# Performance work log

Measured on AMD Instinct MI355X. Metric: run time of the kernel, lower is better.

Reference implementation:

```python
import jax, jax.numpy as jnp
import numpy as np

# hyperparameters (match init_kwargs / AF3 atom transformer)
B, N, C, CP = 1, 2048, 128, 16      # batch, n_atom, c_atom, c_atom_pair
H, D = 4, 32                        # heads, head dim
HD = H * D                          # 128
NB = 3                              # no_blocks
TC = 2 * C                          # n_transition * c_atom
NQ, NK = 32, 128                    # n_query, n_key
INF = 1.0e9


def _ln(x, g=None, b=None):
    m = jnp.mean(x, axis=-1, keepdims=True)
    v = jnp.mean((x - m) ** 2, axis=-1, keepdims=True)
    y = (x - m) * jax.lax.rsqrt(v + 1e-5)
    if g is not None:
        y = y * g
    if b is not None:
        y = y + b
    return y


def _adaln(a, s, gamma, wsig, bsig, wskip):
    # AF3 Algorithm 26: AdaLN(a, s)
    an = _ln(a)                     # no affine
    sn = _ln(s, gamma)              # scale only
    return jax.nn.sigmoid(sn @ wsig + bsig) * an + sn @ wskip


def _neighborhood_beta():
    # compute_neighborhood_mask with create_sparsity_mask=False
    n_center = N // NQ + 1
    centers = (NQ / 2 - 0.5) + jnp.arange(n_center, dtype=jnp.float32) * NQ
    l = jnp.arange(N, dtype=jnp.float32)
    row = (jnp.abs(l[:, None] - centers[None, :]) < NQ / 2).astype(jnp.float32)
    col = (jnp.abs(l[:, None] - centers[None, :]) < NK / 2).astype(jnp.float32)
    beta = row @ col.T              # [N, N], in {0,1} since query windows are disjoint
    return (beta - 1.0) * INF       # 0 where attended, -inf elsewhere


def setup_inputs() -> dict:
    key = jax.random.key(0)
    it = iter(jax.random.split(key, 64))
    def rn(shape, s=0.02):
        return jax.random.normal(next(it), shape, jnp.float32) * s
    inp = dict(
        ql=rn((B, N, C), 1.0),
        cl=rn((B, N, C), 1.0),
        plm=rn((B, N, N, CP), 1.0),
        atom_mask=jnp.ones((B, N), jnp.float32),
        # per-block stacked params, leading dim NB
        attn_gamma=1.0 + rn((NB, C)), attn_wsig=rn((NB, C, C)),
        attn_bsig=rn((NB, C)), attn_wskip=rn((NB, C, C)),
        wq=rn((NB, C, HD)), bq=rn((NB, HD)), wk=rn((NB, C, HD)), wv=rn((NB, C, HD)),
        lnz_g=1.0 + rn((NB, CP)), lnz_b=rn((NB, CP)), w_pair=rn((NB, CP, H)),
        w_gate=rn((NB, C, HD)), w_out=rn((NB, HD, C)),
        w_ao=rn((NB, C, C)), b_ao=rn((NB, C)) - 2.0,
        tr_gamma=1.0 + rn((NB, C)), tr_wsig=rn((NB, C, C)),
        tr_bsig=rn((NB, C)), tr_wskip=rn((NB, C, C)),
        w_t1=rn((NB, C, TC)), w_t2=rn((NB, C, TC)), w_t3=rn((NB, TC, C)),
        w_to=rn((NB, C, C)), b_to=rn((NB, C)) - 2.0,
    )
    return inp


def reference(ql, cl, plm, atom_mask,
              attn_gamma, attn_wsig, attn_bsig, attn_wskip,
              wq, bq, wk, wv, lnz_g, lnz_b, w_pair,
              w_gate, w_out, w_ao, b_ao,
              tr_gamma, tr_wsig, tr_bsig, tr_wskip,
              w_t1, w_t2, w_t3, w_to, b_to):
    beta = _neighborhood_beta()                       # [N, N]
    mask_bias = (atom_mask - 1.0) * INF               # [B, N]
    scale = 1.0 / np.sqrt(D)
    a, s = ql, cl
    for i in range(NB):
        # --- AttentionPairBias with AdaLN (AF3 Alg. 24) ---
        an = _adaln(a, s, attn_gamma[i], attn_wsig[i], attn_bsig[i], attn_wskip[i])
        q = (an @ wq[i] + bq[i]).reshape(B, N, H, D)
        k = (an @ wk[i]).reshape(B, N, H, D)
        v = (an @ wv[i]).reshape(B, N, H, D)
        pb = _ln(plm, lnz_g[i], lnz_b[i]) @ w_pair[i]  # [B, N, N, H]
        logits = (jnp.einsum('bqhd,bkhd->bhqk', q, k) * scale
                  + pb.transpose(0, 3, 1, 2)
                  + beta[None, None]
                  + mask_bias[:, None, None, :])
        attn = jax.nn.softmax(logits, axis=-1)
        o = jnp.einsum('bhqk,bkhd->bqhd', attn, v)
        g = jax.nn.sigmoid(an @ w_gate[i]).reshape(B, N, H, D)
        o = (g * o).reshape(B, N, HD) @ w_out[i]
        b_attn = jax.nn.sigmoid(s @ w_ao[i] + b_ao[i]) * o   # adaLN-zero output gate
        # --- ConditionedTransitionBlock (AF3 Alg. 25) on old a ---
        tn = _adaln(a, s, tr_gamma[i], tr_wsig[i], tr_bsig[i], tr_wskip[i])
        t = jax.nn.silu(tn @ w_t1[i]) * (tn @ w_t2[i])       # SwiGLU
        t = jax.nn.sigmoid(s @ w_to[i] + b_to[i]) * (t @ w_t3[i])
        a = b_attn + t                                       # AF3 Alg. 23
    return a
```

## Files before the change

kernel.cpp:

```cpp
#include <hip/hip_runtime.h>
#include <math.h>

#define NA 2048
#define CD 128
#define NC ((size_t)262144)

typedef unsigned short u16;
typedef short s8v __attribute__((ext_vector_type(8)));
typedef float f4v __attribute__((ext_vector_type(4)));
#define MFMA __builtin_amdgcn_mfma_f32_16x16x32_bf16

__device__ __forceinline__ float sigm(float x) { return 1.f / (1.f + __expf(-x)); }
__device__ __forceinline__ u16 f2bf(float x) {
    unsigned u = __float_as_uint(x);
    u += 0x7fffu + ((u >> 16) & 1u);
    return (u16)(u >> 16);
}
__device__ __forceinline__ float bf2f(u16 h) { return __uint_as_float((unsigned)h << 16); }

__global__ __launch_bounds__(256)
void prep_w(const float* __restrict__ attn_gamma, const float* __restrict__ attn_wsig,
            const float* __restrict__ attn_bsig, const float* __restrict__ attn_wskip,
            const float* __restrict__ wq, const float* __restrict__ wk,
            const float* __restrict__ wv, const float* __restrict__ w_gate,
            const float* __restrict__ w_out, const float* __restrict__ w_ao,
            const float* __restrict__ b_ao,
            const float* __restrict__ tr_gamma, const float* __restrict__ tr_wsig,
            const float* __restrict__ tr_bsig, const float* __restrict__ tr_wskip,
            const float* __restrict__ w_t1, const float* __restrict__ w_t2,
            const float* __restrict__ w_t3, const float* __restrict__ w_to,
            const float* __restrict__ b_to,
            u16* __restrict__ BP1h, u16* __restrict__ BP1l,
            u16* __restrict__ BG1h, u16* __restrict__ BG1l,
            u16* __restrict__ BG2h, u16* __restrict__ BG2l,
            float* __restrict__ Pbias) {
    int e = blockIdx.x * 256 + threadIdx.x;
    if (e >= 835584) {
        int t = e - 835584;
        if (t < 2304) {
            int z = t / 768, rem = t % 768, j = rem >> 7, c = rem & 127;
            float v = 0.f;
            if (j == 0) v = attn_bsig[z * 128 + c];
            else if (j == 2) v = tr_bsig[z * 128 + c];
            else if (j == 4) v = b_ao[z * 128 + c];
            else if (j == 5) v = b_to[z * 128 + c];
            Pbias[t] = v;
        }
        return;
    }
    int z = e / 278528, r = e % 278528;
    float val;
    u16 *dh, *dl;
    size_t dofs;
    if (r < 98304) {
        int c = r >> 7, k = r & 127, seg = c >> 7, cc = c & 127;
        const float* w;
        const float* g = nullptr;
        switch (seg) {
            case 0: w = attn_wsig; g = attn_gamma; break;
            case 1: w = attn_wskip; g = attn_gamma; break;
            case 2: w = tr_wsig; g = tr_gamma; break;
            case 3: w = tr_wskip; g = tr_gamma; break;
            case 4: w = w_ao; break;
            default: w = w_to; break;
        }
        val = w[((size_t)z * 128 + k) * 128 + cc];
        if (g) val *= g[z * 128 + k];
        dh = BP1h; dl = BP1l; dofs = (size_t)z * 98304 + r;
    } else if (r < 229376) {
        int t = r - 98304, c = t >> 7, k = t & 127;
        if (c < 512) {
            int seg = c >> 7, cc = c & 127;
            const float* w = (seg == 0) ? wq : (seg == 1) ? wk : (seg == 2) ? wv : w_gate;
            val = w[((size_t)z * 128 + k) * 128 + cc];
        } else {
            int tt = c - 512;
            const float* w = (tt < 256) ? w_t1 : w_t2;
            val = w[(size_t)z * 32768 + (size_t)k * 256 + (tt & 255)];
        }
        dh = BG1h; dl = BG1l; dofs = (size_t)z * 131072 + t;
    } else {
        int t = r - 229376, c = t / 384, k = t % 384;
        val = (k < 128) ? w_out[((size_t)z * 128 + k) * 128 + c]
                        : w_t3[(size_t)z * 32768 + (size_t)(k - 128) * 128 + c];
        dh = BG2h; dl = BG2l; dofs = (size_t)z * 49152 + t;
    }
    u16 h = f2bf(val);
    dh[dofs] = h;
    dl[dofs] = f2bf(val - bf2f(h));
}

__global__ __launch_bounds__(256)
void pb_kernel(const float* __restrict__ plm, const float* __restrict__ lnz_g,
               const float* __restrict__ lnz_b, const float* __restrict__ w_pair,
               float* __restrict__ pb) {
    __shared__ float gw[3][4][16];
    __shared__ float c0s[3][4];
    int t = threadIdx.x;
    if (t < 12) {
        int i = t >> 2, h = t & 3;
        float c = 0.f;
        for (int cp = 0; cp < 16; ++cp) {
            float wp = w_pair[(i * 16 + cp) * 4 + h];
            gw[i][h][cp] = lnz_g[i * 16 + cp] * wp;
            c += lnz_b[i * 16 + cp] * wp;
        }
        c0s[i][h] = c;
    }
    __syncthreads();
    int c = blockIdx.x;
    int p = blockIdx.y * 256 + t;
    int ql = p >> 7, kl = p & 127;
    int kstart = max(0, c * 32 - 48), kend = min(2048, c * 32 + 80);
    int k = kstart + kl;
    if (k >= kend) {
#pragma unroll
        for (int i = 0; i < 3; ++i)
#pragma unroll
            for (int h = 0; h < 4; ++h)
                pb[((((size_t)i * 64 + c) * 4 + h) * 32 + ql) * 128 + kl] = 0.f;
        return;
    }
    int q = c * 32 + ql;
    const float* row = plm + ((size_t)q * 2048 + (size_t)k) * 16;
    float x[16];
#pragma unroll
    for (int j = 0; j < 4; ++j) {
        float4 v = *(const float4*)(row + j * 4);
        x[j * 4 + 0] = v.x; x[j * 4 + 1] = v.y; x[j * 4 + 2] = v.z; x[j * 4 + 3] = v.w;
    }
    float s = 0.f, sq = 0.f;
#pragma unroll
    for (int cp = 0; cp < 16; ++cp) { s += x[cp]; sq += x[cp] * x[cp]; }
    float mean = s * (1.f / 16.f);
    float var = sq * (1.f / 16.f) - mean * mean;
    float r = 1.f / sqrtf(var + 1e-5f);
    float xn[16];
#pragma unroll
    for (int cp = 0; cp < 16; ++cp) xn[cp] = (x[cp] - mean) * r;
#pragma unroll
    for (int i = 0; i < 3; ++i)
#pragma unroll
        for (int h = 0; h < 4; ++h) {
            float d = c0s[i][h];
#pragma unroll
            for (int cp = 0; cp < 16; ++cp) d = fmaf(xn[cp], gw[i][h][cp], d);
            pb[((((size_t)i * 64 + c) * 4 + h) * 32 + ql) * 128 + kl] = d;
        }
}

__global__ __launch_bounds__(256)
void mf_p1f(const float* __restrict__ cl, const u16* __restrict__ B1h, const u16* __restrict__ B1l,
            const float* __restrict__ Pbias, float* __restrict__ sg) {
    const int r0 = blockIdx.x * 32, chunk = blockIdx.y, z = blockIdx.z;
    __shared__ u16 Ah[32 * 128], Al[32 * 128];
    {
        const int tid = threadIdx.x;
        const int row = tid >> 3, cb = (tid & 7) * 16;
        const float* ar = cl + (size_t)(r0 + row) * CD + cb;
        float x[16];
#pragma unroll
        for (int j = 0; j < 4; ++j) {
            float4 v = *(const float4*)(ar + j * 4);
            x[4 * j] = v.x; x[4 * j + 1] = v.y; x[4 * j + 2] = v.z; x[4 * j + 3] = v.w;
        }
        float s = 0.f, sq = 0.f;
#pragma unroll
        for (int j = 0; j < 16; ++j) { s += x[j]; sq += x[j] * x[j]; }
#pragma unroll
        for (int m = 1; m < 8; m <<= 1) { s += __shfl_xor(s, m); sq += __shfl_xor(sq, m); }
        float mean = s * (1.f / 128.f), var = sq * (1.f / 128.f) - mean * mean;
        float rr = 1.f / sqrtf(var + 1e-5f);
#pragma unroll
        for (int gp = 0; gp < 2; ++gp) {
            u16 hv8[8], lv8[8];
#pragma unroll
            for (int j = 0; j < 8; ++j) {
                float xv = x[gp * 8 + j];
                float val = (chunk < 4) ? (xv - mean) * rr : xv;
                u16 hh = f2bf(val);
                hv8[j] = hh; lv8[j] = f2bf(val - bf2f(hh));
            }
            int g = ((cb >> 3) + gp) ^ (row & 7);
            *(s8v*)(Ah + row * 128 + g * 8) = *(s8v*)hv8;
            *(s8v*)(Al + row * 128 + g * 8) = *(s8v*)lv8;
        }
    }
    __syncthreads();
    const int l = threadIdx.x & 63, w = threadIdx.x >> 6;
    const int lr = l & 15, lq = l >> 4, kg = lq * 8;
    const int c0 = w * 32;
    const u16* Bh = B1h + (size_t)z * 98304 + (size_t)chunk * 16384;
    const u16* Bl = B1l + (size_t)z * 98304 + (size_t)chunk * 16384;
    f4v acc[2][2] = {};
#pragma unroll
    for (int ks = 0; ks < 4; ++ks) {
        int g = (4 * ks + lq) ^ (lr & 7);
        s8v a0h = *(const s8v*)(Ah + lr * 128 + g * 8);
        s8v a1h = *(const s8v*)(Ah + (16 + lr) * 128 + g * 8);
        s8v a0l = *(const s8v*)(Al + lr * 128 + g * 8);
        s8v a1l = *(const s8v*)(Al + (16 + lr) * 128 + g * 8);
        s8v b0h = *(const s8v*)(Bh + (size_t)(c0 + lr) * 128 + ks * 32 + kg);
        s8v b1h = *(const s8v*)(Bh + (size_t)(c0 + 16 + lr) * 128 + ks * 32 + kg);
        s8v b0l = *(const s8v*)(Bl + (size_t)(c0 + lr) * 128 + ks * 32 + kg);
        s8v b1l = *(const s8v*)(Bl + (size_t)(c0 + 16 + lr) * 128 + ks * 32 + kg);
        acc[0][0] = MFMA(a0h, b0h, acc[0][0], 0, 0, 0); acc[0][1] = MFMA(a0h, b1h, acc[0][1], 0, 0, 0);
        acc[1][0] = MFMA(a1h, b0h, acc[1][0], 0, 0, 0); acc[1][1] = MFMA(a1h, b1h, acc[1][1], 0, 0, 0);
        acc[0][0] = MFMA(a0h, b0l, acc[0][0], 0, 0, 0); acc[0][1] = MFMA(a0h, b1l, acc[0][1], 0, 0, 0);
        acc[1][0] = MFMA(a1h, b0l, acc[1][0], 0, 0, 0); acc[1][1] = MFMA(a1h, b1l, acc[1][1], 0, 0, 0);
        acc[0][0] = MFMA(a0l, b0h, acc[0][0], 0, 0, 0); acc[0][1] = MFMA(a0l, b1h, acc[0][1], 0, 0, 0);
        acc[1][0] = MFMA(a1l, b0h, acc[1][0], 0, 0, 0); acc[1][1] = MFMA(a1l, b1h, acc[1][1], 0, 0, 0);
    }
    const bool dosig = (chunk != 1) && (chunk != 3);
    const float* bp = Pbias + (z * 6 + chunk) * 128;
    float* dst = sg + ((size_t)z * 6 + chunk) * NC;
#pragma unroll
    for (int mi = 0; mi < 2; ++mi)
#pragma unroll
        for (int i = 0; i < 4; ++i) {
            int row = r0 + mi * 16 + lq * 4 + i;
#pragma unroll
            for (int ni = 0; ni < 2; ++ni) {
                int col = c0 + ni * 16 + lr;
                float xx = acc[mi][ni][i];
                if (dosig) xx = sigm(xx + bp[col]);
                dst[(size_t)row * CD + col] = xx;
            }
        }
}

__global__ __launch_bounds__(256)
void k1_fused(const float* __restrict__ a, const float* __restrict__ sgi,
              const u16* __restrict__ B1h, const u16* __restrict__ B1l,
              const float* __restrict__ bq,
              u16* __restrict__ qgh, u16* __restrict__ qgl,
              u16* __restrict__ vTh, u16* __restrict__ vTl,
              float* __restrict__ tbuf) {
    const int r0 = blockIdx.x * 32;
    const int y = blockIdx.y;
    __shared__ u16 Ah[32 * 128], Al[32 * 128];
    {
        const int tid = threadIdx.x;
        const int row = tid >> 3, cb = (tid & 7) * 16;
        const float* ar = a + (size_t)(r0 + row) * CD + cb;
        float x[16];
#pragma unroll
        for (int j = 0; j < 4; ++j) {
            float4 v = *(const float4*)(ar + j * 4);
            x[4 * j] = v.x; x[4 * j + 1] = v.y; x[4 * j + 2] = v.z; x[4 * j + 3] = v.w;
        }
        float s = 0.f, sq = 0.f;
#pragma unroll
        for (int j = 0; j < 16; ++j) { s += x[j]; sq += x[j] * x[j]; }
#pragma unroll
        for (int m = 1; m < 8; m <<= 1) { s += __shfl_xor(s, m); sq += __shfl_xor(sq, m); }
        float mean = s * (1.f / 128.f), var = sq * (1.f / 128.f) - mean * mean;
        float rr = 1.f / sqrtf(var + 1e-5f);
        const float* sig = sgi + ((y < 2) ? 0 : 2 * NC) + (size_t)(r0 + row) * CD + cb;
        const float* skp = sgi + ((y < 2) ? NC : 3 * NC) + (size_t)(r0 + row) * CD + cb;
// ... 2 lines not shown
            u16 hv8[8], lv8[8];
#pragma unroll
            for (int j = 0; j < 8; ++j) {
                int jj = gp * 8 + j;
                float ln = (x[jj] - mean) * rr;
                float val = fmaf(sig[jj], ln, skp[jj]);
                u16 hh = f2bf(val);
                hv8[j] = hh; lv8[j] = f2bf(val - bf2f(hh));
            }
            int g = ((cb >> 3) + gp) ^ (row & 7);
            *(s8v*)(Ah + row * 128 + g * 8) = *(s8v*)hv8;
            *(s8v*)(Al + row * 128 + g * 8) = *(s8v*)lv8;
        }
    }
    __syncthreads();
    const int l = threadIdx.x & 63, w = threadIdx.x >> 6;
    const int lr = l & 15, lq = l >> 4, kg = lq * 8;
    const int chunk = 2 * y + (w >> 1);
    const int cbase = (w & 1) * 64;
    f4v acc[2][2][2] = {};
#pragma unroll
    for (int ks = 0; ks < 4; ++ks) {
        int g = (4 * ks + lq) ^ (lr & 7);
        s8v a0h = *(const s8v*)(Ah + lr * 128 + g * 8);
        s8v a1h = *(const s8v*)(Ah + (16 + lr) * 128 + g * 8);
        s8v a0l = *(const s8v*)(Al + lr * 128 + g * 8);
        s8v a1l = *(const s8v*)(Al + (16 + lr) * 128 + g * 8);
#pragma unroll
        for (int t2 = 0; t2 < 2; ++t2) {
            int crow = chunk * 128 + cbase + t2 * 32;
            s8v b0h = *(const s8v*)(B1h + (size_t)(crow + lr) * 128 + ks * 32 + kg);
            s8v b1h = *(const s8v*)(B1h + (size_t)(crow + 16 + lr) * 128 + ks * 32 + kg);
            s8v b0l = *(const s8v*)(B1l + (size_t)(crow + lr) * 128 + ks * 32 + kg);
            s8v b1l = *(const s8v*)(B1l + (size_t)(crow + 16 + lr) * 128 + ks * 32 + kg);
// ... 10 lines not shown
            acc[t2][1][0] = MFMA(a1l, b0h, acc[t2][1][0], 0, 0, 0);
            acc[t2][1][1] = MFMA(a1l, b1h, acc[t2][1][1], 0, 0, 0);
        }
    }
#pragma unroll
    for (int t2 = 0; t2 < 2; ++t2)
#pragma unroll
        for (int mi = 0; mi < 2; ++mi)
#pragma unroll
            for (int i = 0; i < 4; ++i) {
                int row = r0 + mi * 16 + lq * 4 + i;
#pragma unroll
                for (int ni = 0; ni < 2; ++ni) {
                    int gcol = chunk * 128 + cbase + t2 * 32 + ni * 16 + lr;
                    float x = acc[t2][mi][ni][i];
                    if (chunk == 0) x += bq[gcol];
                    if (gcol < 512) {
                        u16 hh = f2bf(x), ll = f2bf(x - bf2f(hh));
                        qgh[(size_t)row * 512 + gcol] = hh;
                        qgl[(size_t)row * 512 + gcol] = ll;
                        if (chunk == 2) {
                            int cv = gcol - 256;
                            vTh[(size_t)cv * 2048 + row] = hh;
                            vTl[(size_t)cv * 2048 + row] = ll;
                        }
                    } else {
                        tbuf[(size_t)row * 512 + (gcol - 512)] = x;
                    }
                }
            }
}

__global__ __launch_bounds__(64)
void attn_mfma(const u16* __restrict__ qgh, const u16* __restrict__ qgl,
               const u16* __restrict__ vTh, const u16* __restrict__ vTl,
               const float* __restrict__ pb, const float* __restrict__ atom_mask,
               u16* __restrict__ ogh, u16* __restrict__ ogl) {
    const int c = blockIdx.x, h = blockIdx.y;
    const int l = threadIdx.x;
    const int kstart = max(0, c * 32 - 48);
    const int kend = min(2048, c * 32 + 80);
    const int nk = kend - kstart;
    const int lr = l & 15, lq = l >> 4, kg = lq * 8;

    __shared__ u16 Pls[32 * 128];

    s8v qfh[2], qfl[2];
#pragma unroll
    for (int mi = 0; mi < 2; ++mi) {
        size_t qb = (size_t)(c * 32 + mi * 16 + lr) * 512 + h * 32 + kg;
        qfh[mi] = *(const s8v*)(qgh + qb);
        qfl[mi] = *(const s8v*)(qgl + qb);
    }
    f4v lac[2][8] = {};
#pragma unroll
    for (int kt = 0; kt < 8; ++kt) {
        int krow = min(kstart + kt * 16 + lr, 2047);
        size_t kb = (size_t)krow * 512 + 128 + h * 32 + kg;
        s8v bh = *(const s8v*)(qgh + kb);
        s8v bl = *(const s8v*)(qgl + kb);
        lac[0][kt] = MFMA(qfh[0], bh, lac[0][kt], 0, 0, 0);
        lac[1][kt] = MFMA(qfh[1], bh, lac[1][kt], 0, 0, 0);
        lac[0][kt] = MFMA(qfh[0], bl, lac[0][kt], 0, 0, 0);
        lac[1][kt] = MFMA(qfh[1], bl, lac[1][kt], 0, 0, 0);
        lac[0][kt] = MFMA(qfl[0], bh, lac[0][kt], 0, 0, 0);
        lac[1][kt] = MFMA(qfl[1], bh, lac[1][kt], 0, 0, 0);
    }
    float mb8[8];
#pragma unroll
    for (int kt = 0; kt < 8; ++kt) {
        int kl = kt * 16 + lr;
        mb8[kt] = (kl < nk) ? (atom_mask[kstart + kl] - 1.f) * 1.0e9f : 0.f;
    }
    const float scale = 0.17677669529663687f;
    const float* pbp = pb + (size_t)((c * 4 + h) * 32) * 128;
    float inv_s[2][4];
#pragma unroll
    for (int mi = 0; mi < 2; ++mi)
#pragma unroll
        for (int i = 0; i < 4; ++i) {
            const int rl = mi * 16 + lq * 4 + i;
            float lg[8];
#pragma unroll
            for (int kt = 0; kt < 8; ++kt) {
                int kl = kt * 16 + lr;
                float v = -1e30f;
                if (kl < nk) v = fmaf(lac[mi][kt][i], scale, pbp[(size_t)rl * 128 + kl] + mb8[kt]);
                lg[kt] = v;
            }
            float m = lg[0];
#pragma unroll
            for (int kt = 1; kt < 8; ++kt) m = fmaxf(m, lg[kt]);
#pragma unroll
            for (int msk = 1; msk < 16; msk <<= 1) m = fmaxf(m, __shfl_xor(m, msk));
            float ssum = 0.f;
#pragma unroll
            for (int kt = 0; kt < 8; ++kt) {
                float p = __expf(lg[kt] - m);
                u16 p16 = f2bf(p);
                ssum += bf2f(p16);
                int kl = kt * 16 + lr;
                int g = (kl >> 3) ^ (rl & 7);
                Pls[rl * 128 + g * 8 + (kl & 7)] = p16;
            }
#pragma unroll
            for (int msk = 1; msk < 16; msk <<= 1) ssum += __shfl_xor(ssum, msk);
            inv_s[mi][i] = 1.f / ssum;
        }
    __syncthreads();
    f4v oac[2][2] = {};
#pragma unroll
    for (int ks = 0; ks < 4; ++ks) {
        s8v pA[2];
#pragma unroll
        for (int mi = 0; mi < 2; ++mi) {
            int row = mi * 16 + lr;
            int g = (4 * ks + lq) ^ (row & 7);
            pA[mi] = *(const s8v*)(Pls + row * 128 + g * 8);
        }
#pragma unroll
        for (int ct = 0; ct < 2; ++ct) {
            size_t vb = (size_t)(h * 32 + ct * 16 + lr) * 2048 + kstart + ks * 32 + kg;
            s8v vh = *(const s8v*)(vTh + vb);
            s8v vl = *(const s8v*)(vTl + vb);
            oac[0][ct] = MFMA(pA[0], vh, oac[0][ct], 0, 0, 0);
            oac[1][ct] = MFMA(pA[1], vh, oac[1][ct], 0, 0, 0);
            oac[0][ct] = MFMA(pA[0], vl, oac[0][ct], 0, 0, 0);
            oac[1][ct] = MFMA(pA[1], vl, oac[1][ct], 0, 0, 0);
        }
    }
#pragma unroll
    for (int mi = 0; mi < 2; ++mi)
#pragma unroll
        for (int ct = 0; ct < 2; ++ct)
#pragma unroll
            for (int i = 0; i < 4; ++i) {
                int rl = mi * 16 + lq * 4 + i;
                int row = c * 32 + rl;
                int d = ct * 16 + lr;
                float o = oac[mi][ct][i] * inv_s[mi][i];
                size_t gidx = (size_t)row * 512 + 384 + h * 32 + d;
                float g = bf2f(qgh[gidx]) + bf2f(qgl[gidx]);
                float v = o * sigm(g);
                u16 hh = f2bf(v);
                size_t oi = (size_t)row * 128 + h * 32 + d;
                ogh[oi] = hh;
                ogl[oi] = f2bf(v - bf2f(hh));
            }
}

__global__ __launch_bounds__(256)
void k3_fused(const float* __restrict__ tbuf,
              const u16* __restrict__ ogh, const u16* __restrict__ ogl,
              const u16* __restrict__ B2h, const u16* __restrict__ B2l,
              const float* __restrict__ sg4, const float* __restrict__ sg5,
              float* __restrict__ dst) {
    const int r0 = blockIdx.x * 32;
    __shared__ u16 Sh[32 * 256], Sl[32 * 256];
    {
        const int tid = threadIdx.x;
        const int row = tid >> 3, cb = (tid & 7) * 32;
#pragma unroll
        for (int u = 0; u < 4; ++u) {
            int colb = cb + u * 8;
            const float* t1 = tbuf + (size_t)(r0 + row) * 512 + colb;
            const float* t2 = t1 + 256;
            u16 hv8[8], lv8[8];
#pragma unroll
            for (int j2 = 0; j2 < 2; ++j2) {
                float4 x1 = *(const float4*)(t1 + j2 * 4);
                float4 x2 = *(const float4*)(t2 + j2 * 4);
                float sv[4];
                sv[0] = x1.x * sigm(x1.x) * x2.x;
                sv[1] = x1.y * sigm(x1.y) * x2.y;
                sv[2] = x1.z * sigm(x1.z) * x2.z;
                sv[3] = x1.w * sigm(x1.w) * x2.w;
#pragma unroll
                for (int j = 0; j < 4; ++j) {
                    u16 hh = f2bf(sv[j]);
                    hv8[j2 * 4 + j] = hh;
                    lv8[j2 * 4 + j] = f2bf(sv[j] - bf2f(hh));
                }
            }
            int g = (colb >> 3) ^ (row & 7);
            *(s8v*)(Sh + row * 256 + g * 8) = *(s8v*)hv8;
            *(s8v*)(Sl + row * 256 + g * 8) = *(s8v*)lv8;
        }
    }
    __syncthreads();
    const int l = threadIdx.x & 63, w = threadIdx.x >> 6;
    const int lr = l & 15, lq = l >> 4, kg = lq * 8;
    const int c0 = w * 32;
    f4v ac1[2][2] = {}, ac2[2][2] = {};
#pragma unroll
    for (int ks = 0; ks < 4; ++ks) {
        s8v a0h = *(const s8v*)(ogh + (size_t)(r0 + lr) * 128 + ks * 32 + kg);
        s8v a1h = *(const s8v*)(ogh + (size_t)(r0 + 16 + lr) * 128 + ks * 32 + kg);
        s8v a0l = *(const s8v*)(ogl + (size_t)(r0 + lr) * 128 + ks * 32 + kg);
        s8v a1l = *(const s8v*)(ogl + (size_t)(r0 + 16 + lr) * 128 + ks * 32 + kg);
        s8v b0h = *(const s8v*)(B2h + (size_t)(c0 + lr) * 384 + ks * 32 + kg);
        s8v b1h = *(const s8v*)(B2h + (size_t)(c0 + 16 + lr) * 384 + ks * 32 + kg);
        s8v b0l = *(const s8v*)(B2l + (size_t)(c0 + lr) * 384 + ks * 32 + kg);
        s8v b1l = *(const s8v*)(B2l + (size_t)(c0 + 16 + lr) * 384 + ks * 32 + kg);
        ac1[0][0] = MFMA(a0h, b0h, ac1[0][0], 0, 0, 0); ac1[0][1] = MFMA(a0h, b1h, ac1[0][1], 0, 0, 0);
        ac1[1][0] = MFMA(a1h, b0h, ac1[1][0], 0, 0, 0); ac1[1][1] = MFMA(a1h, b1h, ac1[1][1], 0, 0, 0);
        ac1[0][0] = MFMA(a0h, b0l, ac1[0][0], 0, 0, 0); ac1[0][1] = MFMA(a0h, b1l, ac1[0][1], 0, 0, 0);
        ac1[1][0] = MFMA(a1h, b0l, ac1[1][0], 0, 0, 0); ac1[1][1] = MFMA(a1h, b1l, ac1[1][1], 0, 0, 0);
        ac1[0][0] = MFMA(a0l, b0h, ac1[0][0], 0, 0, 0); ac1[0][1] = MFMA(a0l, b1h, ac1[0][1], 0, 0, 0);
        ac1[1][0] = MFMA(a1l, b0h, ac1[1][0], 0, 0, 0); ac1[1][1] = MFMA(a1l, b1h, ac1[1][1], 0, 0, 0);
    }
#pragma unroll
    for (int ks = 0; ks < 8; ++ks) {
        int g = (4 * ks + lq) ^ (lr & 7);
        s8v a0h = *(const s8v*)(Sh + lr * 256 + g * 8);
// ... 11 lines not shown
        ac2[0][0] = MFMA(a0l, b0h, ac2[0][0], 0, 0, 0); ac2[0][1] = MFMA(a0l, b1h, ac2[0][1], 0, 0, 0);
        ac2[1][0] = MFMA(a1l, b0h, ac2[1][0], 0, 0, 0); ac2[1][1] = MFMA(a1l, b1h, ac2[1][1], 0, 0, 0);
    }
#pragma unroll
    for (int mi = 0; mi < 2; ++mi)
#pragma unroll
        for (int i = 0; i < 4; ++i) {
            int row = r0 + mi * 16 + lq * 4 + i;
#pragma unroll
            for (int ni = 0; ni < 2; ++ni) {
                int col = c0 + ni * 16 + lr;
                size_t idx = (size_t)row * CD + col;
                dst[idx] = sg4[idx] * ac1[mi][ni][i] + sg5[idx] * ac2[mi][ni][i];
            }
        }
}

extern "C" void kernel_launch(void* const* d_in, const int* in_sizes, int n_in,
                              void* d_out, int out_size, void* d_ws, size_t ws_size,
                              hipStream_t stream) {
    const float* ql = (const float*)d_in[0];
    const float* cl = (const float*)d_in[1];
    const float* plm = (const float*)d_in[2];
    const float* atom_mask = (const float*)d_in[3];
    const float* attn_gamma = (const float*)d_in[4];
    const float* attn_wsig = (const float*)d_in[5];
    const float* attn_bsig = (const float*)d_in[6];
    const float* attn_wskip = (const float*)d_in[7];
    const float* wq = (const float*)d_in[8];
    const float* bq = (const float*)d_in[9];
    const float* wk = (const float*)d_in[10];
    const float* wv = (const float*)d_in[11];
    const float* lnz_g = (const float*)d_in[12];
    const float* lnz_b = (const float*)d_in[13];
    const float* w_pair = (const float*)d_in[14];
    const float* w_gate = (const float*)d_in[15];
    const float* w_out = (const float*)d_in[16];
    const float* w_ao = (const float*)d_in[17];
    const float* b_ao = (const float*)d_in[18];
    const float* tr_gamma = (const float*)d_in[19];
    const float* tr_wsig = (const float*)d_in[20];
    const float* tr_bsig = (const float*)d_in[21];
    const float* tr_wskip = (const float*)d_in[22];
    const float* w_t1 = (const float*)d_in[23];
    const float* w_t2 = (const float*)d_in[24];
    const float* w_t3 = (const float*)d_in[25];
    const float* w_to = (const float*)d_in[26];
    const float* b_to = (const float*)d_in[27];
    float* out = (float*)d_out;
    float* ws = (float*)d_ws;

    float* sg = ws;
    float* tbuf = ws + 18 * NC;
    float* pb = ws + 22 * NC;
    float* a_buf = ws + 34 * NC;
    float* Pbias = ws + 35 * NC;
    u16* us = (u16*)(ws + 36 * NC);
    u16* qgh = us;
    u16* qgl = qgh + 4 * NC;
    u16* ogh = qgl + 4 * NC;
    u16* ogl = ogh + NC;
    u16* vTh = ogl + NC;
    u16* vTl = vTh + NC + 128;
    u16* BP1h = vTl + NC + 128;
    u16* BP1l = BP1h + 294912;
    u16* BG1h = BP1l + 294912;
    u16* BG1l = BG1h + 393216;
    u16* BG2h = BG1l + 393216;
    u16* BG2l = BG2h + 147456;

    size_t used_bytes = (size_t)36 * NC * 4 +
                        ((size_t)12 * NC + 256 + 2 * 294912 + 2 * 393216 + 2 * 147456) * 2;
    hipMemsetAsync(d_ws, 0, used_bytes, stream);

    prep_w<<<3273, 256, 0, stream>>>(attn_gamma, attn_wsig, attn_bsig, attn_wskip,
        wq, wk, wv, w_gate, w_out, w_ao, b_ao,
        tr_gamma, tr_wsig, tr_bsig, tr_wskip,
        w_t1, w_t2, w_t3, w_to, b_to,
        BP1h, BP1l, BG1h, BG1l, BG2h, BG2l, Pbias);
    pb_kernel<<<dim3(64, 16), 256, 0, stream>>>(plm, lnz_g, lnz_b, w_pair, pb);
    mf_p1f<<<dim3(64, 6, 3), 256, 0, stream>>>(cl, BP1h, BP1l, Pbias, sg);

    for (int i = 0; i < 3; ++i) {
        const float* a_cur = (i == 0) ? ql : a_buf;
        float* sgi = sg + (size_t)i * 6 * NC;
        k1_fused<<<dim3(64, 4), 256, 0, stream>>>(a_cur, sgi,
            BG1h + (size_t)i * 131072, BG1l + (size_t)i * 131072,
            bq + (size_t)i * 128, qgh, qgl, vTh, vTl, tbuf);
        attn_mfma<<<dim3(64, 4), 64, 0, stream>>>(qgh, qgl, vTh, vTl,
            pb + (size_t)i * 64 * 4 * 32 * 128, atom_mask, ogh, ogl);
        float* dst = (i == 2) ? out : a_buf;
        k3_fused<<<64, 256, 0, stream>>>(tbuf, ogh, ogl,
            BG2h + (size_t)i * 49152, BG2l + (size_t)i * 49152,
            sgi + 4 * NC, sgi + 5 * NC, dst);
    }
}
```

Baseline: 191.2 us.

## Merge pb and p1 prep into one launch and split attention across two waves

Device functions now take a shared parameter struct. The pair-bias and cl-projection kernels are merged into one combined grid launch, so one launch is saved and the two independent jobs can overlap. The attention kernel now runs 128 threads, with each wave owning one 16-row query tile, which doubles the waves per block. It also keeps a low-order bf16 residual for the softmax probabilities, which adds precision and an extra LDS buffer plus more MFMA work.

```diff
diff --git a/kernel.cpp b/kernel.cpp
--- a/kernel.cpp
+++ b/kernel.cpp
@@ -18,33 +18,27 @@
 }
 __device__ __forceinline__ float bf2f(u16 h) { return __uint_as_float((unsigned)h << 16); }
 
-__global__ __launch_bounds__(256)
-void prep_w(const float* __restrict__ attn_gamma, const float* __restrict__ attn_wsig,
-            const float* __restrict__ attn_bsig, const float* __restrict__ attn_wskip,
-            const float* __restrict__ wq, const float* __restrict__ wk,
-            const float* __restrict__ wv, const float* __restrict__ w_gate,
-            const float* __restrict__ w_out, const float* __restrict__ w_ao,
-            const float* __restrict__ b_ao,
-            const float* __restrict__ tr_gamma, const float* __restrict__ tr_wsig,
-            const float* __restrict__ tr_bsig, const float* __restrict__ tr_wskip,
-            const float* __restrict__ w_t1, const float* __restrict__ w_t2,
-            const float* __restrict__ w_t3, const float* __restrict__ w_to,
-            const float* __restrict__ b_to,
-            u16* __restrict__ BP1h, u16* __restrict__ BP1l,
-            u16* __restrict__ BG1h, u16* __restrict__ BG1l,
-            u16* __restrict__ BG2h, u16* __restrict__ BG2l,
-            float* __restrict__ Pbias) {
-    int e = blockIdx.x * 256 + threadIdx.x;
+struct MegaP {
+    const float *ql, *cl, *plm, *atom_mask;
+    const float *attn_gamma, *attn_wsig, *attn_bsig, *attn_wskip;
+    const float *wq, *bq, *wk, *wv, *lnz_g, *lnz_b, *w_pair, *w_gate, *w_out, *w_ao, *b_ao;
+    const float *tr_gamma, *tr_wsig, *tr_bsig, *tr_wskip, *w_t1, *w_t2, *w_t3, *w_to, *b_to;
+    float *out, *sg, *tbuf, *pb, *a_buf, *Pbias;
+    u16 *qgh, *qgl, *ogh, *ogl, *vTh, *vTl, *BP1h, *BP1l, *BG1h, *BG1l, *BG2h, *BG2l;
+};
+
+
+__device__ __forceinline__ void dev_prep(const MegaP& P, int e) {
     if (e >= 835584) {
         int t = e - 835584;
         if (t < 2304) {
             int z = t / 768, rem = t % 768, j = rem >> 7, c = rem & 127;
             float v = 0.f;
-            if (j == 0) v = attn_bsig[z * 128 + c];
-            else if (j == 2) v = tr_bsig[z * 128 + c];
-            else if (j == 4) v = b_ao[z * 128 + c];
-            else if (j == 5) v = b_to[z * 128 + c];
-            Pbias[t] = v;
+            if (j == 0) v = P.attn_bsig[z * 128 + c];
+            else if (j == 2) v = P.tr_bsig[z * 128 + c];
+            else if (j == 4) v = P.b_ao[z * 128 + c];
+            else if (j == 5) v = P.b_to[z * 128 + c];
+            P.Pbias[t] = v;
         }
         return;
     }
@@ -57,60 +51,56 @@
         const float* w;
         const float* g = nullptr;
         switch (seg) {
-            case 0: w = attn_wsig; g = attn_gamma; break;
-            case 1: w = attn_wskip; g = attn_gamma; break;
-            case 2: w = tr_wsig; g = tr_gamma; break;
-            case 3: w = tr_wskip; g = tr_gamma; break;
-            case 4: w = w_ao; break;
-            default: w = w_to; break;
+            case 0: w = P.attn_wsig; g = P.attn_gamma; break;
+            case 1: w = P.attn_wskip; g = P.attn_gamma; break;
+            case 2: w = P.tr_wsig; g = P.tr_gamma; break;
+            case 3: w = P.tr_wskip; g = P.tr_gamma; break;
+            case 4: w = P.w_ao; break;
+            default: w = P.w_to; break;
         }
         val = w[((size_t)z * 128 + k) * 128 + cc];
         if (g) val *= g[z * 128 + k];
-        dh = BP1h; dl = BP1l; dofs = (size_t)z * 98304 + r;
+        dh = P.BP1h; dl = P.BP1l; dofs = (size_t)z * 98304 + r;
     } else if (r < 229376) {
         int t = r - 98304, c = t >> 7, k = t & 127;
         if (c < 512) {
             int seg = c >> 7, cc = c & 127;
-            const float* w = (seg == 0) ? wq : (seg == 1) ? wk : (seg == 2) ? wv : w_gate;
+            const float* w = (seg == 0) ? P.wq : (seg == 1) ? P.wk : (seg == 2) ? P.wv : P.w_gate;
             val = w[((size_t)z * 128 + k) * 128 + cc];
         } else {
             int tt = c - 512;
-            const float* w = (tt < 256) ? w_t1 : w_t2;
+            const float* w = (tt < 256) ? P.w_t1 : P.w_t2;
             val = w[(size_t)z * 32768 + (size_t)k * 256 + (tt & 255)];
         }
-        dh = BG1h; dl = BG1l; dofs = (size_t)z * 131072 + t;
+        dh = P.BG1h; dl = P.BG1l; dofs = (size_t)z * 131072 + t;
     } else {
         int t = r - 229376, c = t / 384, k = t % 384;
-        val = (k < 128) ? w_out[((size_t)z * 128 + k) * 128 + c]
-                        : w_t3[(size_t)z * 32768 + (size_t)(k - 128) * 128 + c];
-        dh = BG2h; dl = BG2l; dofs = (size_t)z * 49152 + t;
+        val = (k < 128) ? P.w_out[((size_t)z * 128 + k) * 128 + c]
+                        : P.w_t3[(size_t)z * 32768 + (size_t)(k - 128) * 128 + c];
+        dh = P.BG2h; dl = P.BG2l; dofs = (size_t)z * 49152 + t;
     }
     u16 h = f2bf(val);
     dh[dofs] = h;
     dl[dofs] = f2bf(val - bf2f(h));
 }
 
-__global__ __launch_bounds__(256)
-void pb_kernel(const float* __restrict__ plm, const float* __restrict__ lnz_g,
-               const float* __restrict__ lnz_b, const float* __restrict__ w_pair,
-               float* __restrict__ pb) {
-    __shared__ float gw[3][4][16];
-    __shared__ float c0s[3][4];
-    int t = threadIdx.x;
-    if (t < 12) {
-        int i = t >> 2, h = t & 3;
+__device__ __forceinline__ void dev_pb_fold(const MegaP& P, float (*gw)[4][16], float (*c0s)[4], int tid) {
+    if (tid < 12) {
+        int i = tid >> 2, h = tid & 3;
         float c = 0.f;
         for (int cp = 0; cp < 16; ++cp) {
-            float wp = w_pair[(i * 16 + cp) * 4 + h];
-            gw[i][h][cp] = lnz_g[i * 16 + cp] * wp;
-            c += lnz_b[i * 16 + cp] * wp;
+            float wp = P.w_pair[(i * 16 + cp) * 4 + h];
+            gw[i][h][cp] = P.lnz_g[i * 16 + cp] * wp;
+            c += P.lnz_b[i * 16 + cp] * wp;
         }
         c0s[i][h] = c;
     }
-    __syncthreads();
-    int c = blockIdx.x;
-    int p = blockIdx.y * 256 + t;
-    int ql = p >> 7, kl = p & 127;
+}
+
+__device__ __forceinline__ void dev_pb(const MegaP& P, float (*gw)[4][16], float (*c0s)[4],
+                                       int c, int yy, int tid) {
+    int p = yy * 256 + tid;
+    int ql_ = p >> 7, kl = p & 127;
     int kstart = max(0, c * 32 - 48), kend = min(2048, c * 32 + 80);
     int k = kstart + kl;
     if (k >= kend) {
@@ -118,11 +108,11 @@
         for (int i = 0; i < 3; ++i)
 #pragma unroll
             for (int h = 0; h < 4; ++h)
-                pb[((((size_t)i * 64 + c) * 4 + h) * 32 + ql) * 128 + kl] = 0.f;
+                P.pb[((((size_t)i * 64 + c) * 4 + h) * 32 + ql_) * 128 + kl] = 0.f;
         return;
     }
-    int q = c * 32 + ql;
-    const float* row = plm + ((size_t)q * 2048 + (size_t)k) * 16;
+    int q = c * 32 + ql_;
+    const float* row = P.plm + ((size_t)q * 2048 + (size_t)k) * 16;
     float x[16];
 #pragma unroll
     for (int j = 0; j < 4; ++j) {
@@ -145,19 +135,16 @@
             float d = c0s[i][h];
 #pragma unroll
             for (int cp = 0; cp < 16; ++cp) d = fmaf(xn[cp], gw[i][h][cp], d);
-            pb[((((size_t)i * 64 + c) * 4 + h) * 32 + ql) * 128 + kl] = d;
-        }
-}
-
-__global__ __launch_bounds__(256)
-void mf_p1f(const float* __restrict__ cl, const u16* __restrict__ B1h, const u16* __restrict__ B1l,
-            const float* __restrict__ Pbias, float* __restrict__ sg) {
-    const int r0 = blockIdx.x * 32, chunk = blockIdx.y, z = blockIdx.z;
-    __shared__ u16 Ah[32 * 128], Al[32 * 128];
+            P.pb[((((size_t)i * 64 + c) * 4 + h) * 32 + ql_) * 128 + kl] = d;
+        }
+}
+
+__device__ __forceinline__ void dev_p1f(const MegaP& P, int x_, int chunk, int z, int tid,
+                                        u16* Ah, u16* Al) {
+    const int r0 = x_ * 32;
     {
-        const int tid = threadIdx.x;
         const int row = tid >> 3, cb = (tid & 7) * 16;
-        const float* ar = cl + (size_t)(r0 + row) * CD + cb;
+        const float* ar = P.cl + (size_t)(r0 + row) * CD + cb;
         float x[16];
 #pragma unroll
         for (int j = 0; j < 4; ++j) {
@@ -187,11 +174,11 @@
         }
     }
     __syncthreads();
-    const int l = threadIdx.x & 63, w = threadIdx.x >> 6;
+    const int l = tid & 63, wv_ = tid >> 6;
     const int lr = l & 15, lq = l >> 4, kg = lq * 8;
-    const int c0 = w * 32;
-    const u16* Bh = B1h + (size_t)z * 98304 + (size_t)chunk * 16384;
-    const u16* Bl = B1l + (size_t)z * 98304 + (size_t)chunk * 16384;
+    const int c0 = wv_ * 32;
+    const u16* Bh = P.BP1h + (size_t)z * 98304 + (size_t)chunk * 16384;
+    const u16* Bl = P.BP1l + (size_t)z * 98304 + (size_t)chunk * 16384;
     f4v acc[2][2] = {};
 #pragma unroll
     for (int ks = 0; ks < 4; ++ks) {
@@ -212,8 +199,8 @@
         acc[1][0] = MFMA(a1l, b0h, acc[1][0], 0, 0, 0); acc[1][1] = MFMA(a1l, b1h, acc[1][1], 0, 0, 0);
     }
     const bool dosig = (chunk != 1) && (chunk != 3);
-    const float* bp = Pbias + (z * 6 + chunk) * 128;
-    float* dst = sg + ((size_t)z * 6 + chunk) * NC;
+    const float* bp = P.Pbias + (z * 6 + chunk) * 128;
+    float* dst = P.sg + ((size_t)z * 6 + chunk) * NC;
 #pragma unroll
     for (int mi = 0; mi < 2; ++mi)
 #pragma unroll
@@ -227,22 +214,19 @@
                 dst[(size_t)row * CD + col] = xx;
             }
         }
-}
-
-__global__ __launch_bounds__(256)
-void k1_fused(const float* __restrict__ a, const float* __restrict__ sgi,
-              const u16* __restrict__ B1h, const u16* __restrict__ B1l,
-              const float* __restrict__ bq,
-              u16* __restrict__ qgh, u16* __restrict__ qgl,
-              u16* __restrict__ vTh, u16* __restrict__ vTl,
-              float* __restrict__ tbuf) {
-    const int r0 = blockIdx.x * 32;
-    const int y = blockIdx.y;
-    __shared__ u16 Ah[32 * 128], Al[32 * 128];
+    __syncthreads();
+}
+
+__device__ __forceinline__ void dev_k1(const MegaP& P, int ib, int r0, int y, int tid,
+                                       u16* Ah, u16* Al) {
+    const float* a_cur = (ib == 0) ? P.ql : P.a_buf;
+    const float* sgi = P.sg + (size_t)ib * 6 * NC;
+    const u16* B1h = P.BG1h + (size_t)ib * 131072;
+    const u16* B1l = P.BG1l + (size_t)ib * 131072;
+    const float* bqz = P.bq + (size_t)ib * 128;
     {
-        const int tid = threadIdx.x;
         const int row = tid >> 3, cb = (tid & 7) * 16;
-        const float* ar = a + (size_t)(r0 + row) * CD + cb;
+        const float* ar = a_cur + (size_t)(r0 + row) * CD + cb;
         float x[16];
 #pragma unroll
         for (int j = 0; j < 4; ++j) {
@@ -275,10 +259,10 @@
         }
     }
     __syncthreads();
-    const int l = threadIdx.x & 63, w = threadIdx.x >> 6;
+    const int l = tid & 63, wv_ = tid >> 6;
     const int lr = l & 15, lq = l >> 4, kg = lq * 8;
-    const int chunk = 2 * y + (w >> 1);
-    const int cbase = (w & 1) * 64;
+    const int chunk = 2 * y + (wv_ >> 1);
+    const int cbase = (wv_ & 1) * 64;
     f4v acc[2][2][2] = {};
 #pragma unroll
     for (int ks = 0; ks < 4; ++ks) {
@@ -319,69 +303,59 @@
                 for (int ni = 0; ni < 2; ++ni) {
                     int gcol = chunk * 128 + cbase + t2 * 32 + ni * 16 + lr;
                     float x = acc[t2][mi][ni][i];
-                    if (chunk == 0) x += bq[gcol];
+                    if (chunk == 0) x += bqz[gcol];
                     if (gcol < 512) {
                         u16 hh = f2bf(x), ll = f2bf(x - bf2f(hh));
-                        qgh[(size_t)row * 512 + gcol] = hh;
-                        qgl[(size_t)row * 512 + gcol] = ll;
+                        P.qgh[(size_t)row * 512 + gcol] = hh;
+                        P.qgl[(size_t)row * 512 + gcol] = ll;
                         if (chunk == 2) {
                             int cv = gcol - 256;
-                            vTh[(size_t)cv * 2048 + row] = hh;
-                            vTl[(size_t)cv * 2048 + row] = ll;
+                            P.vTh[(size_t)cv * 2048 + row] = hh;
+                            P.vTl[(size_t)cv * 2048 + row] = ll;
                         }
                     } else {
-                        tbuf[(size_t)row * 512 + (gcol - 512)] = x;
+                        P.tbuf[(size_t)row * 512 + (gcol - 512)] = x;
                     }
                 }
             }
-}
-
-__global__ __launch_bounds__(64)
-void attn_mfma(const u16* __restrict__ qgh, const u16* __restrict__ qgl,
-               const u16* __restrict__ vTh, const u16* __restrict__ vTl,
-               const float* __restrict__ pb, const float* __restrict__ atom_mask,
-               u16* __restrict__ ogh, u16* __restrict__ ogl) {
-    const int c = blockIdx.x, h = blockIdx.y;
-    const int l = threadIdx.x;
+    __syncthreads();
+}
+
+__device__ __forceinline__ void dev_attn(const MegaP& P, int ib, int c, int h,
+                                         int tid, bool act, int mi, u16* Pls, u16* Pll) {
+    const int l = tid & 63;
     const int kstart = max(0, c * 32 - 48);
     const int kend = min(2048, c * 32 + 80);
     const int nk = kend - kstart;
     const int lr = l & 15, lq = l >> 4, kg = lq * 8;
-
-    __shared__ u16 Pls[32 * 128];
-
-    s8v qfh[2], qfl[2];
-#pragma unroll
-    for (int mi = 0; mi < 2; ++mi) {
-        size_t qb = (size_t)(c * 32 + mi * 16 + lr) * 512 + h * 32 + kg;
-        qfh[mi] = *(const s8v*)(qgh + qb);
-        qfl[mi] = *(const s8v*)(qgl + qb);
-    }
-    f4v lac[2][8] = {};
-#pragma unroll
-    for (int kt = 0; kt < 8; ++kt) {
-        int krow = min(kstart + kt * 16 + lr, 2047);
-        size_t kb = (size_t)krow * 512 + 128 + h * 32 + kg;
-        s8v bh = *(const s8v*)(qgh + kb);
-        s8v bl = *(const s8v*)(qgl + kb);
-        lac[0][kt] = MFMA(qfh[0], bh, lac[0][kt], 0, 0, 0);
-        lac[1][kt] = MFMA(qfh[1], bh, lac[1][kt], 0, 0, 0);
-        lac[0][kt] = MFMA(qfh[0], bl, lac[0][kt], 0, 0, 0);
-        lac[1][kt] = MFMA(qfh[1], bl, lac[1][kt], 0, 0, 0);
-        lac[0][kt] = MFMA(qfl[0], bh, lac[0][kt], 0, 0, 0);
-        lac[1][kt] = MFMA(qfl[1], bh, lac[1][kt], 0, 0, 0);
-    }
-    float mb8[8];
-#pragma unroll
-    for (int kt = 0; kt < 8; ++kt) {
-        int kl = kt * 16 + lr;
-        mb8[kt] = (kl < nk) ? (atom_mask[kstart + kl] - 1.f) * 1.0e9f : 0.f;
-    }
-    const float scale = 0.17677669529663687f;
-    const float* pbp = pb + (size_t)((c * 4 + h) * 32) * 128;
-    float inv_s[2][4];
-#pragma unroll
-    for (int mi = 0; mi < 2; ++mi)
+    const float* pbp = P.pb + (size_t)ib * 4 * NC + (size_t)((c * 4 + h) * 32) * 128;
+    f4v oac[2] = {};
+    float inv_s[4];
+    if (act) {
+        s8v qfh, qfl;
+        {
+            size_t qb = (size_t)(c * 32 + mi * 16 + lr) * 512 + h * 32 + kg;
+            qfh = *(const s8v*)(P.qgh + qb);
+            qfl = *(const s8v*)(P.qgl + qb);
+        }
+        f4v lac[8] = {};
+#pragma unroll
+        for (int kt = 0; kt < 8; ++kt) {
+            int krow = min(kstart + kt * 16 + lr, 2047);
+            size_t kb = (size_t)krow * 512 + 128 + h * 32 + kg;
+            s8v bh = *(const s8v*)(P.qgh + kb);
+            s8v bl = *(const s8v*)(P.qgl + kb);
+            lac[kt] = MFMA(qfh, bh, lac[kt], 0, 0, 0);
+            lac[kt] = MFMA(qfh, bl, lac[kt], 0, 0, 0);
+            lac[kt] = MFMA(qfl, bh, lac[kt], 0, 0, 0);
+        }
+        float mb8[8];
+#pragma unroll
+        for (int kt = 0; kt < 8; ++kt) {
+            int kl = kt * 16 + lr;
+            mb8[kt] = (kl < nk) ? (P.atom_mask[kstart + kl] - 1.f) * 1.0e9f : 0.f;
+        }
+        const float scale = 0.17677669529663687f;
 #pragma unroll
         for (int i = 0; i < 4; ++i) {
             const int rl = mi * 16 + lq * 4 + i;
@@ -390,7 +364,7 @@
             for (int kt = 0; kt < 8; ++kt) {
                 int kl = kt * 16 + lr;
                 float v = -1e30f;
-                if (kl < nk) v = fmaf(lac[mi][kt][i], scale, pbp[(size_t)rl * 128 + kl] + mb8[kt]);
+                if (kl < nk) v = fmaf(lac[kt][i], scale, pbp[(size_t)rl * 128 + kl] + mb8[kt]);
                 lg[kt] = v;
             }
             float m = lg[0];
@@ -402,40 +376,38 @@
 #pragma unroll
             for (int kt = 0; kt < 8; ++kt) {
                 float p = __expf(lg[kt] - m);
+                ssum += p;
                 u16 p16 = f2bf(p);
-                ssum += bf2f(p16);
                 int kl = kt * 16 + lr;
                 int g = (kl >> 3) ^ (rl & 7);
                 Pls[rl * 128 + g * 8 + (kl & 7)] = p16;
+                Pll[rl * 128 + g * 8 + (kl & 7)] = f2bf(p - bf2f(p16));
             }
 #pragma unroll
             for (int msk = 1; msk < 16; msk <<= 1) ssum += __shfl_xor(ssum, msk);
-            inv_s[mi][i] = 1.f / ssum;
-        }
+            inv_s[i] = 1.f / ssum;
+        }
+    }
     __syncthreads();
-    f4v oac[2][2] = {};
-#pragma unroll
-    for (int ks = 0; ks < 4; ++ks) {
-        s8v pA[2];
-#pragma unroll
-        for (int mi = 0; mi < 2; ++mi) {
-            int row = mi * 16 + lr;
-            int g = (4 * ks + lq) ^ (row & 7);
-            pA[mi] = *(const s8v*)(Pls + row * 128 + g * 8);
-        }
-#pragma unroll
-        for (int ct = 0; ct < 2; ++ct) {
-            size_t vb = (size_t)(h * 32 + ct * 16 + lr) * 2048 + kstart + ks * 32 + kg;
-            s8v vh = *(const s8v*)(vTh + vb);
-            s8v vl = *(const s8v*)(vTl + vb);
-            oac[0][ct] = MFMA(pA[0], vh, oac[0][ct], 0, 0, 0);
-            oac[1][ct] = MFMA(pA[1], vh, oac[1][ct], 0, 0, 0);
-            oac[0][ct] = MFMA(pA[0], vl, oac[0][ct], 0, 0, 0);
-            oac[1][ct] = MFMA(pA[1], vl, oac[1][ct], 0, 0, 0);
-        }
-    }
-#pragma unroll
-    for (int mi = 0; mi < 2; ++mi)
+    if (act) {
+#pragma unroll
+        for (int ks = 0; ks < 4; ++ks) {
+            int prow = mi * 16 + lr;
+            int g = (4 * ks + lq) ^ (prow & 7);
+            s8v pA = *(const s8v*)(Pls + prow * 128 + g * 8);
+            s8v pAl = *(const s8v*)(Pll + prow * 128 + g * 8);
+            int kcol = kstart + ks * 32 + kg;
+            if (kcol > 2040) kcol = 0;
+#pragma unroll
+            for (int ct = 0; ct < 2; ++ct) {
+                size_t vb = (size_t)(h * 32 + ct * 16 + lr) * 2048 + kcol;
+                s8v vh = *(const s8v*)(P.vTh + vb);
+                s8v vl = *(const s8v*)(P.vTl + vb);
+                oac[ct] = MFMA(pA, vh, oac[ct], 0, 0, 0);
+                oac[ct] = MFMA(pA, vl, oac[ct], 0, 0, 0);
+                oac[ct] = MFMA(pAl, vh, oac[ct], 0, 0, 0);
+            }
+        }
 #pragma unroll
         for (int ct = 0; ct < 2; ++ct)
 #pragma unroll
@@ -443,32 +415,31 @@
                 int rl = mi * 16 + lq * 4 + i;
                 int row = c * 32 + rl;
                 int d = ct * 16 + lr;
-                float o = oac[mi][ct][i] * inv_s[mi][i];
+                float o = oac[ct][i] * inv_s[i];
                 size_t gidx = (size_t)row * 512 + 384 + h * 32 + d;
-                float g = bf2f(qgh[gidx]) + bf2f(qgl[gidx]);
+                float g = bf2f(P.qgh[gidx]) + bf2f(P.qgl[gidx]);
                 float v = o * sigm(g);
                 u16 hh = f2bf(v);
                 size_t oi = (size_t)row * 128 + h * 32 + d;
-                ogh[oi] = hh;
-                ogl[oi] = f2bf(v - bf2f(hh));
-            }
-}
-
-__global__ __launch_bounds__(256)
-void k3_fused(const float* __restrict__ tbuf,
-              const u16* __restrict__ ogh, const u16* __restrict__ ogl,
-              const u16* __restrict__ B2h, const u16* __restrict__ B2l,
-              const float* __restrict__ sg4, const float* __restrict__ sg5,
-              float* __restrict__ dst) {
-    const int r0 = blockIdx.x * 32;
-    __shared__ u16 Sh[32 * 256], Sl[32 * 256];
+                P.ogh[oi] = hh;
+                P.ogl[oi] = f2bf(v - bf2f(hh));
+            }
+    }
+}
+
+__device__ __forceinline__ void dev_k3(const MegaP& P, int ib, int r0, int tid,
+                                       u16* Sh, u16* Sl) {
+    const u16* B2h = P.BG2h + (size_t)ib * 49152;
+    const u16* B2l = P.BG2l + (size_t)ib * 49152;
+    const float* sg4 = P.sg + (size_t)ib * 6 * NC + 4 * NC;
+    const float* sg5 = P.sg + (size_t)ib * 6 * NC + 5 * NC;
+    float* dst = (ib == 2) ? P.out : P.a_buf;
     {
-        const int tid = threadIdx.x;
         const int row = tid >> 3, cb = (tid & 7) * 32;
 #pragma unroll
         for (int u = 0; u < 4; ++u) {
             int colb = cb + u * 8;
-            const float* t1 = tbuf + (size_t)(r0 + row) * 512 + colb;
+            const float* t1 = P.tbuf + (size_t)(r0 + row) * 512 + colb;
             const float* t2 = t1 + 256;
             u16 hv8[8], lv8[8];
 #pragma unroll
@@ -493,16 +464,16 @@
         }
     }
     __syncthreads();
-    const int l = threadIdx.x & 63, w = threadIdx.x >> 6;
+    const int l = tid & 63, wv_ = tid >> 6;
     const int lr = l & 15, lq = l >> 4, kg = lq * 8;
-    const int c0 = w * 32;
+    const int c0 = wv_ * 32;
     f4v ac1[2][2] = {}, ac2[2][2] = {};
 #pragma unroll
     for (int ks = 0; ks < 4; ++ks) {
-        s8v a0h = *(const s8v*)(ogh + (size_t)(r0 + lr) * 128 + ks * 32 + kg);
-        s8v a1h = *(const s8v*)(ogh + (size_t)(r0 + 16 + lr) * 128 + ks * 32 + kg);
-        s8v a0l = *(const s8v*)(ogl + (size_t)(r0 + lr) * 128 + ks * 32 + kg);
-        s8v a1l = *(const s8v*)(ogl + (size_t)(r0 + 16 + lr) * 128 + ks * 32 + kg);
+        s8v a0h = *(const s8v*)(P.ogh + (size_t)(r0 + lr) * 128 + ks * 32 + kg);
+        s8v a1h = *(const s8v*)(P.ogh + (size_t)(r0 + 16 + lr) * 128 + ks * 32 + kg);
+        s8v a0l = *(const s8v*)(P.ogl + (size_t)(r0 + lr) * 128 + ks * 32 + kg);
+        s8v a1l = *(const s8v*)(P.ogl + (size_t)(r0 + 16 + lr) * 128 + ks * 32 + kg);
         s8v b0h = *(const s8v*)(B2h + (size_t)(c0 + lr) * 384 + ks * 32 + kg);
         s8v b1h = *(const s8v*)(B2h + (size_t)(c0 + 16 + lr) * 384 + ks * 32 + kg);
         s8v b0l = *(const s8v*)(B2l + (size_t)(c0 + lr) * 384 + ks * 32 + kg);
@@ -544,84 +515,109 @@
                 dst[idx] = sg4[idx] * ac1[mi][ni][i] + sg5[idx] * ac2[mi][ni][i];
             }
         }
+    __syncthreads();
+}
+
+
+__global__ __launch_bounds__(256) void prep_w_k(MegaP P) {
+    dev_prep(P, blockIdx.x * 256 + threadIdx.x);
+}
+
+__global__ __launch_bounds__(256) void combo_pp(MegaP P) {
+    int bx = blockIdx.x;
+    if (bx < 1152) {
+        __shared__ u16 Ah[32 * 128], Al[32 * 128];
+        int x_ = bx & 63, rem = bx >> 6;
+        dev_p1f(P, x_, rem % 6, rem / 6, threadIdx.x, Ah, Al);
+    } else {
+        __shared__ float gw[3][4][16];
+        __shared__ float c0s[3][4];
+        dev_pb_fold(P, gw, c0s, threadIdx.x);
+        __syncthreads();
+        int pt = bx - 1152;
+        dev_pb(P, gw, c0s, pt & 63, pt >> 6, threadIdx.x);
+    }
+}
+
+__global__ __launch_bounds__(256) void k1_k(MegaP P, int ib) {
+    __shared__ u16 Ah[32 * 128], Al[32 * 128];
+    dev_k1(P, ib, blockIdx.x * 32, blockIdx.y, threadIdx.x, Ah, Al);
+}
+
+__global__ __launch_bounds__(128) void attn_k(MegaP P, int ib) {
+    __shared__ u16 Pls[32 * 128], Pll[32 * 128];
+    dev_attn(P, ib, blockIdx.x, blockIdx.y, threadIdx.x, true, threadIdx.x >> 6, Pls, Pll);
+}
+
+__global__ __launch_bounds__(256) void k3_k(MegaP P, int ib) {
+    __shared__ u16 Sh[32 * 256], Sl[32 * 256];
+    dev_k3(P, ib, blockIdx.x * 32, threadIdx.x, Sh, Sl);
 }
 
 extern "C" void kernel_launch(void* const* d_in, const int* in_sizes, int n_in,
                               void* d_out, int out_size, void* d_ws, size_t ws_size,
                               hipStream_t stream) {
-    const float* ql = (const float*)d_in[0];
-    const float* cl = (const float*)d_in[1];
-    const float* plm = (const float*)d_in[2];
-    const float* atom_mask = (const float*)d_in[3];
-    const float* attn_gamma = (const float*)d_in[4];
-    const float* attn_wsig = (const float*)d_in[5];
-    const float* attn_bsig = (const float*)d_in[6];
-    const float* attn_wskip = (const float*)d_in[7];
-    const float* wq = (const float*)d_in[8];
-    const float* bq = (const float*)d_in[9];
-    const float* wk = (const float*)d_in[10];
-    const float* wv = (const float*)d_in[11];
-    const float* lnz_g = (const float*)d_in[12];
-    const float* lnz_b = (const float*)d_in[13];
-    const float* w_pair = (const float*)d_in[14];
-    const float* w_gate = (const float*)d_in[15];
-    const float* w_out = (const float*)d_in[16];
-    const float* w_ao = (const float*)d_in[17];
-    const float* b_ao = (const float*)d_in[18];
-    const float* tr_gamma = (const float*)d_in[19];
-    const float* tr_wsig = (const float*)d_in[20];
-    const float* tr_bsig = (const float*)d_in[21];
-    const float* tr_wskip = (const float*)d_in[22];
-    const float* w_t1 = (const float*)d_in[23];
-    const float* w_t2 = (const float*)d_in[24];
-    const float* w_t3 = (const float*)d_in[25];
-    const float* w_to = (const float*)d_in[26];
-    const float* b_to = (const float*)d_in[27];
-    float* out = (float*)d_out;
     float* ws = (float*)d_ws;
 
-    float* sg = ws;
-    float* tbuf = ws + 18 * NC;
-    float* pb = ws + 22 * NC;
-    float* a_buf = ws + 34 * NC;
-    float* Pbias = ws + 35 * NC;
+    MegaP P;
+    P.ql = (const float*)d_in[0];
+    P.cl = (const float*)d_in[1];
+    P.plm = (const float*)d_in[2];
+    P.atom_mask = (const float*)d_in[3];
+    P.attn_gamma = (const float*)d_in[4];
+    P.attn_wsig = (const float*)d_in[5];
+    P.attn_bsig = (const float*)d_in[6];
+    P.attn_wskip = (const float*)d_in[7];
+    P.wq = (const float*)d_in[8];
+    P.bq = (const float*)d_in[9];
+    P.wk = (const float*)d_in[10];
+    P.wv = (const float*)d_in[11];
+    P.lnz_g = (const float*)d_in[12];
+    P.lnz_b = (const float*)d_in[13];
+    P.w_pair = (const float*)d_in[14];
+    P.w_gate = (const float*)d_in[15];
+    P.w_out = (const float*)d_in[16];
+    P.w_ao = (const float*)d_in[17];
+    P.b_ao = (const float*)d_in[18];
+    P.tr_gamma = (const float*)d_in[19];
+    P.tr_wsig = (const float*)d_in[20];
+    P.tr_bsig = (const float*)d_in[21];
+    P.tr_wskip = (const float*)d_in[22];
+    P.w_t1 = (const float*)d_in[23];
+    P.w_t2 = (const float*)d_in[24];
+    P.w_t3 = (const float*)d_in[25];
+    P.w_to = (const float*)d_in[26];
+    P.b_to = (const float*)d_in[27];
+    P.out = (float*)d_out;
+
+    P.sg = ws;
+    P.tbuf = ws + 18 * NC;
+    P.pb = ws + 22 * NC;
+    P.a_buf = ws + 34 * NC;
+    P.Pbias = ws + 35 * NC;
     u16* us = (u16*)(ws + 36 * NC);
-    u16* qgh = us;
-    u16* qgl = qgh + 4 * NC;
-    u16* ogh = qgl + 4 * NC;
-    u16* ogl = ogh + NC;
-    u16* vTh = ogl + NC;
-    u16* vTl = vTh + NC + 128;
-    u16* BP1h = vTl + NC + 128;
-    u16* BP1l = BP1h + 294912;
-    u16* BG1h = BP1l + 294912;
-    u16* BG1l = BG1h + 393216;
-    u16* BG2h = BG1l + 393216;
-    u16* BG2l = BG2h + 147456;
+    P.qgh = us;
+    P.qgl = P.qgh + 4 * NC;
+    P.ogh = P.qgl + 4 * NC;
+    P.ogl = P.ogh + NC;
+    P.vTh = P.ogl + NC;
+    P.vTl = P.vTh + NC + 128;
+    P.BP1h = P.vTl + NC + 128;
+    P.BP1l = P.BP1h + 294912;
+    P.BG1h = P.BP1l + 294912;
+    P.BG1l = P.BG1h + 393216;
+    P.BG2h = P.BG1l + 393216;
+    P.BG2l = P.BG2h + 147456;
 
     size_t used_bytes = (size_t)36 * NC * 4 +
                         ((size_t)12 * NC + 256 + 2 * 294912 + 2 * 393216 + 2 * 147456) * 2;
     hipMemsetAsync(d_ws, 0, used_bytes, stream);
 
-    prep_w<<<3273, 256, 0, stream>>>(attn_gamma, attn_wsig, attn_bsig, attn_wskip,
-        wq, wk, wv, w_gate, w_out, w_ao, b_ao,
-        tr_gamma, tr_wsig, tr_bsig, tr_wskip,
-        w_t1, w_t2, w_t3, w_to, b_to,
-        BP1h, BP1l, BG1h, BG1l, BG2h, BG2l, Pbias);
-    pb_kernel<<<dim3(64, 16), 256, 0, stream>>>(plm, lnz_g, lnz_b, w_pair, pb);
-    mf_p1f<<<dim3(64, 6, 3), 256, 0, stream>>>(cl, BP1h, BP1l, Pbias, sg);
-
-    for (int i = 0; i < 3; ++i) {
-        const float* a_cur = (i == 0) ? ql : a_buf;
-        float* sgi = sg + (size_t)i * 6 * NC;
-        k1_fused<<<dim3(64, 4), 256, 0, stream>>>(a_cur, sgi,
-            BG1h + (size_t)i * 131072, BG1l + (size_t)i * 131072,
-            bq + (size_t)i * 128, qgh, qgl, vTh, vTl, tbuf);
-        attn_mfma<<<dim3(64, 4), 64, 0, stream>>>(qgh, qgl, vTh, vTl,
-            pb + (size_t)i * 64 * 4 * 32 * 128, atom_mask, ogh, ogl);
-        float* dst = (i == 2) ? out : a_buf;
-        k3_fused<<<64, 256, 0, stream>>>(tbuf, ogh, ogl,
-            BG2h + (size_t)i * 49152, BG2l + (size_t)i * 49152,
-            sgi + 4 * NC, sgi + 5 * NC, dst);
-    }
-}
+    prep_w_k<<<3273, 256, 0, stream>>>(P);
+    combo_pp<<<2176, 256, 0, stream>>>(P);
+    for (int ib = 0; ib < 3; ++ib) {
+        k1_k<<<dim3(64, 4), 256, 0, stream>>>(P, ib);
+        attn_k<<<dim3(64, 4), 128, 0, stream>>>(P, ib);
+        k3_k<<<64, 256, 0, stream>>>(P, ib);
+    }
+}
```

After: 189.0 us. About the same (-1.1%).
